# Kernel tuning notes

Measured on AMD Instinct MI355X. Metric: run time of the kernel, lower is better.

Reference implementation:

```python
import jax, jax.numpy as jnp
import numpy as np

B, S, D = 4, 2048, 1024
H, DK, DV, DFF = 16, 64, 64, 4096
EPS = 1e-5


def layer_norm(x, g, b):
    mu = jnp.mean(x, axis=-1, keepdims=True)
    var = jnp.mean((x - mu) ** 2, axis=-1, keepdims=True)
    return (x - mu) * jax.lax.rsqrt(var + EPS) * g + b


def setup_inputs() -> dict:
    key = jax.random.key(0)
    ks = jax.random.split(key, 12)
    s = lambda fan_in: 1.0 / np.sqrt(fan_in)
    return {
        "x": jax.random.normal(ks[0], (B, S, D), dtype=jnp.float32),
        # per-head projections stacked: [H, D, DK/DV] (x @ W layout)
        "Wq": jax.random.normal(ks[1], (H, D, DK), dtype=jnp.float32) * s(D),
        "Wk": jax.random.normal(ks[2], (H, D, DK), dtype=jnp.float32) * s(D),
        "Wv": jax.random.normal(ks[3], (H, D, DV), dtype=jnp.float32) * s(D),
        "Wo": jax.random.normal(ks[4], (H * DV, D), dtype=jnp.float32) * s(H * DV),
        "ln1_g": jnp.ones((D,), dtype=jnp.float32),
        "ln1_b": jnp.zeros((D,), dtype=jnp.float32),
        "W1": jax.random.normal(ks[5], (D, DFF), dtype=jnp.float32) * s(D),
        "b1": jnp.zeros((DFF,), dtype=jnp.float32),
        "W2": jax.random.normal(ks[6], (DFF, D), dtype=jnp.float32) * s(DFF),
        "b2": jnp.zeros((D,), dtype=jnp.float32),
        "ln2_g": jnp.ones((D,), dtype=jnp.float32),
        "ln2_b": jnp.zeros((D,), dtype=jnp.float32),
    }


def reference(x, Wq, Wk, Wv, Wo, ln1_g, ln1_b, W1, b1, W2, b2, ln2_g, ln2_b):
    # --- multi-head causal self-attention (all heads vectorized) ---
    q = jnp.einsum("bsd,hdk->bhsk", x, Wq)
    k = jnp.einsum("bsd,hdk->bhsk", x, Wk)
    v = jnp.einsum("bsd,hdv->bhsv", x, Wv)
    # NOTE: original scales by 1/sqrt(x.shape[-1]) == 1/sqrt(d_model)
    scale = 1.0 / np.sqrt(D).astype(np.float32)
    scores = jnp.einsum("bhsk,bhtk->bhst", q, k) * scale  # [B,H,S,S]
    causal = jnp.tril(jnp.ones((S, S), dtype=bool))
    scores = jnp.where(causal, scores, -jnp.inf)
    attn = jax.nn.softmax(scores, axis=-1)
    ctx = jnp.einsum("bhst,bhtv->bhsv", attn, v)  # [B,H,S,DV]
    # concat heads (head-major last dim, matches torch.cat order)
    ctx = ctx.transpose(0, 2, 1, 3).reshape(B, S, H * DV)
    attn_out = ctx @ Wo  # [B,S,D]
    # Sublayer 1 (dropout is identity in eval)
    h1 = layer_norm(x + attn_out, ln1_g, ln1_b)
    # --- FFN ---
    ff = jax.nn.relu(h1 @ W1 + b1) @ W2 + b2
    # Sublayer 2
    return layer_norm(h1 + ff, ln2_g, ln2_b)
```

## Files before the change

kernel.cpp:

```cpp
#include <hip/hip_runtime.h>

#define DEV __device__ __forceinline__

using f16x8 = _Float16 __attribute__((ext_vector_type(8)));
using f16x4 = _Float16 __attribute__((ext_vector_type(4)));
using f32x4 = float __attribute__((ext_vector_type(4)));

DEV f32x4 mfma16(f16x8 a, f16x8 b, f32x4 c) {
    return __builtin_amdgcn_mfma_f32_16x16x32_f16(a, b, c, 0, 0, 0);
}

DEV void gload16(const void* g, void* l) {
    __builtin_amdgcn_global_load_lds(
        (const __attribute__((address_space(1))) void*)g,
        (__attribute__((address_space(3))) void*)l, 16, 0, 0);
}

template <int MODE>
__global__ __launch_bounds__(256, 2) void gemm_bt(
    const _Float16* __restrict__ A, const _Float16* __restrict__ Bt,
    int M, int N, int K,
    const float* __restrict__ ep0, const float* __restrict__ ep1,
    void* __restrict__ o0, void* __restrict__ o1, void* __restrict__ o2)
{
    __shared__ __align__(16) _Float16 As[128 * 64];
    __shared__ __align__(16) _Float16 Bs[128 * 64];
    const int tid  = threadIdx.x;
    const int wave = tid >> 6, lane = tid & 63;
    const int l16  = lane & 15, g = lane >> 4;
    const int m0 = blockIdx.x * 128, n0 = blockIdx.y * 128;
    const int wm = (wave >> 1) * 64, wn = (wave & 1) * 64;

    f32x4 acc[4][4] = {};

    for (int kt = 0; kt < K; kt += 64) {
#pragma unroll
        for (int it = 0; it < 4; ++it) {
            const int off  = it * 4096 + tid * 16;
            const int row  = off >> 7;
            const int colb = (off & 127) ^ ((row & 7) << 4);
            gload16(A + (size_t)(m0 + row) * K + kt + (colb >> 1), (char*)As + off);
        }
#pragma unroll
        for (int it = 0; it < 4; ++it) {
            const int off  = it * 4096 + tid * 16;
            const int row  = off >> 7;
            const int colb = (off & 127) ^ ((row & 7) << 4);
            gload16(Bt + (size_t)(n0 + row) * K + kt + (colb >> 1), (char*)Bs + off);
        }
        __syncthreads();
#pragma unroll
        for (int kk = 0; kk < 2; ++kk) {
            f16x8 af[4], bfv[4];
#pragma unroll
            for (int i = 0; i < 4; ++i) {
                const int ar = wm + i * 16 + l16;
                const int cb = ((kk * 32 + g * 8) << 1) ^ ((ar & 7) << 4);
                af[i] = *(const f16x8*)((const char*)As + (ar << 7) + cb);
            }
#pragma unroll
            for (int j = 0; j < 4; ++j) {
                const int br = wn + j * 16 + l16;
                const int cb = ((kk * 32 + g * 8) << 1) ^ ((br & 7) << 4);
                bfv[j] = *(const f16x8*)((const char*)Bs + (br << 7) + cb);
            }
#pragma unroll
            for (int i = 0; i < 4; ++i)
#pragma unroll
                for (int j = 0; j < 4; ++j)
                    acc[i][j] = mfma16(af[i], bfv[j], acc[i][j]);
        }
        __syncthreads();
    }

#pragma unroll
    for (int i = 0; i < 4; ++i) {
#pragma unroll
        for (int j = 0; j < 4; ++j) {
#pragma unroll
            for (int r = 0; r < 4; ++r) {
                const int m = m0 + wm + i * 16 + g * 4 + r;
                const int n = n0 + wn + j * 16 + l16;
                const float val = acc[i][j][r];
                if constexpr (MODE == 0) {
                    const int b = m >> 11, s = m & 2047;
                    const int which = n >> 10, hh = (n >> 6) & 15, dd = n & 63;
                    const size_t bh = (size_t)(b * 16 + hh);
                    const _Float16 hv = (_Float16)val;
                    if (which == 0)      ((_Float16*)o0)[(bh * 2048 + s) * 64 + dd] = hv;
                    else if (which == 1) ((_Float16*)o1)[(bh * 2048 + s) * 64 + dd] = hv;
                    else                 ((_Float16*)o2)[(bh * 64 + dd) * 2048 + s] = hv;
                } else if constexpr (MODE == 1) {
                    const size_t idx = (size_t)m * N + n;
                    ((float*)o0)[idx] = val + ep0[idx];
                } else if constexpr (MODE == 2) {
                    float v = val + ep0[n];
                    ((_Float16*)o0)[(size_t)m * N + n] = (_Float16)(v > 0.f ? v : 0.f);
                } else {
                    const size_t idx = (size_t)m * N + n;
                    ((float*)o0)[idx] = val + ep0[n] + ep1[idx];
                }
            }
        }
    }
}

__global__ __launch_bounds__(256, 4) void attn_kernel(
    const _Float16* __restrict__ Q, const _Float16* __restrict__ Kb,
    const _Float16* __restrict__ Vt, _Float16* __restrict__ ctx)
{
    __shared__ __align__(16) _Float16 Ks[64 * 64];
    __shared__ __align__(16) _Float16 Vs[64 * 64];
    __shared__ __align__(16) _Float16 P_lds[4][16][72];
    __shared__ __align__(16) float f_lds[4][16];
    const int tid = threadIdx.x;
    const int w = tid >> 6, lane = tid & 63;
    const int l16 = lane & 15, g = lane >> 4;
    const int bh = blockIdx.y;
    const int b = bh >> 4, h = bh & 15;
    const int tA = blockIdx.x;

    const _Float16* Kh = Kb + (size_t)bh * 2048 * 64;
    const _Float16* Vh = Vt + (size_t)bh * 64 * 2048;
    const int swl = (l16 & 7) << 4;

    for (int half = 0; half < 2; ++half) {
        const int T = half ? (31 - tA) : tA;
        const int qbase = T * 64 + w * 16;
        const int qg = qbase + l16;

        const _Float16* qrow = Q + ((size_t)bh * 2048 + qg) * 64;
        const f16x8 qf0 = *(const f16x8*)(qrow + g * 8);
        const f16x8 qf1 = *(const f16x8*)(qrow + 32 + g * 8);

        f32x4 cacc[4] = {};
        float m_run = -INFINITY, l_run = 0.f;

        for (int kt = 0; kt <= T; ++kt) {
            const int kb0 = kt * 64;
#pragma unroll
            for (int it = 0; it < 2; ++it) {
                const int off  = it * 4096 + tid * 16;
                const int row  = off >> 7;
                const int colb = (off & 127) ^ ((row & 7) << 4);
                gload16(Kh + (size_t)(kb0 + row) * 64 + (colb >> 1), (char*)Ks + off);
            }
#pragma unroll
            for (int it = 0; it < 2; ++it) {
                const int off  = it * 4096 + tid * 16;
                const int row  = off >> 7;
                const int colb = (off & 127) ^ ((row & 7) << 4);
                gload16(Vh + (size_t)row * 2048 + kb0 + (colb >> 1), (char*)Vs + off);
            }
            __syncthreads();

            f32x4 st[4] = {{0.f,0.f,0.f,0.f},{0.f,0.f,0.f,0.f},
                           {0.f,0.f,0.f,0.f},{0.f,0.f,0.f,0.f}};
            __builtin_amdgcn_s_setprio(1);
#pragma unroll
            for (int s = 0; s < 4; ++s) {
                const char* kr = (const char*)Ks + (16 * s + l16) * 128;
                const f16x8 klo = *(const f16x8*)(kr + ((g * 16) ^ swl));
                const f16x8 khi = *(const f16x8*)(kr + ((64 + g * 16) ^ swl));
                st[s] = mfma16(klo, qf0, st[s]);
                st[s] = mfma16(khi, qf1, st[s]);
            }
            __builtin_amdgcn_s_setprio(0);

            const bool maskt = (kt == T);
            float sv[16];
            float tmax = -INFINITY;
#pragma unroll
            for (int s = 0; s < 4; ++s)
#pragma unroll
                for (int r = 0; r < 4; ++r) {
                    const int kg = kb0 + s * 16 + g * 4 + r;
                    float v = st[s][r] * 0.03125f;
                    v = (!maskt || kg <= qg) ? v : -INFINITY;
                    sv[s * 4 + r] = v;
                    tmax = fmaxf(tmax, v);
                }
            tmax = fmaxf(tmax, __shfl_xor(tmax, 16));
            tmax = fmaxf(tmax, __shfl_xor(tmax, 32));
            const float m_new = fmaxf(m_run, tmax);
            const float alpha = __expf(m_run - m_new);
            float tsum = 0.f;
            f16x4 p[4];
#pragma unroll
            for (int s = 0; s < 4; ++s)
#pragma unroll
                for (int r = 0; r < 4; ++r) {
                    const float e = __expf(sv[s * 4 + r] - m_new);
                    tsum += e;
                    p[s][r] = (_Float16)e;
                }
            tsum += __shfl_xor(tsum, 16);
            tsum += __shfl_xor(tsum, 32);
            l_run = l_run * alpha + tsum;
            m_run = m_new;

#pragma unroll
            for (int s = 0; s < 4; ++s)
                *(f16x4*)&P_lds[w][l16][s * 16 + g * 4] = p[s];
            if (g == 0) f_lds[w][l16] = alpha;

            const f32x4 al  = *(const f32x4*)&f_lds[w][g * 4];
            const f16x8 pf0 = *(const f16x8*)&P_lds[w][l16][g * 8];
            const f16x8 pf1 = *(const f16x8*)&P_lds[w][l16][32 + g * 8];
            __builtin_amdgcn_s_setprio(1);
#pragma unroll
            for (int jt = 0; jt < 4; ++jt) {
                const char* vr = (const char*)Vs + (jt * 16 + l16) * 128;
                const f16x8 vlo = *(const f16x8*)(vr + ((g * 16) ^ swl));
                const f16x8 vhi = *(const f16x8*)(vr + ((64 + g * 16) ^ swl));
#pragma unroll
                for (int r = 0; r < 4; ++r) cacc[jt][r] *= al[r];
                cacc[jt] = mfma16(pf0, vlo, cacc[jt]);
                cacc[jt] = mfma16(pf1, vhi, cacc[jt]);
            }
            __builtin_amdgcn_s_setprio(0);
            __syncthreads();
        }

        if (g == 0) f_lds[w][l16] = 1.f / l_run;
        const f32x4 il = *(const f32x4*)&f_lds[w][g * 4];
#pragma unroll
        for (int jt = 0; jt < 4; ++jt)
#pragma unroll
            for (int r = 0; r < 4; ++r)
                ctx[((size_t)b * 2048 + qbase + g * 4 + r) * 1024 + h * 64 + jt * 16 + l16]
                    = (_Float16)(cacc[jt][r] * il[r]);
    }
}

__global__ __launch_bounds__(256) void ln_kernel(
    const float* __restrict__ in, const float* __restrict__ gam, const float* __restrict__ bet,
    float* __restrict__ out32, _Float16* __restrict__ out16)
{
    const int row = blockIdx.x, tid = threadIdx.x;
    const float4 x = ((const float4*)(in + (size_t)row * 1024))[tid];
    float s  = x.x + x.y + x.z + x.w;
    float s2 = x.x * x.x + x.y * x.y + x.z * x.z + x.w * x.w;
#pragma unroll
    for (int o = 32; o > 0; o >>= 1) {
        s  += __shfl_xor(s, o);
        s2 += __shfl_xor(s2, o);
    }
    __shared__ float red[8];
    if ((tid & 63) == 0) { red[tid >> 6] = s; red[4 + (tid >> 6)] = s2; }
    __syncthreads();
    const float S  = red[0] + red[1] + red[2] + red[3];
    const float S2 = red[4] + red[5] + red[6] + red[7];
    const float mu = S * (1.f / 1024.f);
    const float ir = rsqrtf(S2 * (1.f / 1024.f) - mu * mu + 1e-5f);
    const float4 gv = ((const float4*)gam)[tid];
    const float4 bv = ((const float4*)bet)[tid];
    float4 o;
    o.x = (x.x - mu) * ir * gv.x + bv.x;
    o.y = (x.y - mu) * ir * gv.y + bv.y;
    o.z = (x.z - mu) * ir * gv.z + bv.z;
    o.w = (x.w - mu) * ir * gv.w + bv.w;
    if (out32) ((float4*)(out32 + (size_t)row * 1024))[tid] = o;
    if (out16) {
        f16x4 h;
        h[0] = (_Float16)o.x; h[1] = (_Float16)o.y; h[2] = (_Float16)o.z; h[3] = (_Float16)o.w;
        *(f16x4*)(out16 + (size_t)row * 1024 + tid * 4) = h;
    }
}

__global__ __launch_bounds__(256) void cast_f16(const float* __restrict__ in,
                                                _Float16* __restrict__ out, int n4)
{
    const int i = blockIdx.x * 256 + threadIdx.x;
    if (i < n4) {
        const float4 v = ((const float4*)in)[i];
        f16x4 h;
        h[0] = (_Float16)v.x; h[1] = (_Float16)v.y; h[2] = (_Float16)v.z; h[3] = (_Float16)v.w;
        ((f16x4*)out)[i] = h;
    }
}

__global__ __launch_bounds__(256) void transpose_cast(const float* __restrict__ src,
                                                      _Float16* __restrict__ dst, int K, int N)
{
    __shared__ float tile[64][65];
    const int n0 = blockIdx.x * 64, k0 = blockIdx.y * 64;
    const int tid = threadIdx.x;
#pragma unroll
    for (int it = 0; it < 16; ++it) {
        const int idx = it * 256 + tid;
        const int r = idx >> 6, c = idx & 63;
        tile[r][c] = src[(size_t)(k0 + r) * N + n0 + c];
    }
    __syncthreads();
#pragma unroll
    for (int it = 0; it < 16; ++it) {
        const int idx = it * 256 + tid;
        const int r = idx >> 6, c = idx & 63;
        dst[(size_t)(n0 + r) * K + k0 + c] = (_Float16)tile[c][r];
    }
}

__global__ __launch_bounds__(256) void pack_qkv_w(const float* __restrict__ Wq,
                                                  const float* __restrict__ Wk,
                                                  const float* __restrict__ Wv,
                                                  _Float16* __restrict__ dst)
{
    __shared__ float tile[64][65];
    const int n0 = blockIdx.x * 64, d0 = blockIdx.y * 64;
    const int which = n0 >> 10, hh = (n0 >> 6) & 15;
    const float* W = which == 0 ? Wq : (which == 1 ? Wk : Wv);
    const int tid = threadIdx.x;
#pragma unroll
    for (int it = 0; it < 16; ++it) {
        const int idx = it * 256 + tid;
        const int r = idx >> 6, c = idx & 63;
        tile[r][c] = W[((size_t)hh * 1024 + d0 + r) * 64 + c];
    }
    __syncthreads();
#pragma unroll
    for (int it = 0; it < 16; ++it) {
        const int idx = it * 256 + tid;
        const int r = idx >> 6, c = idx & 63;
        dst[(size_t)(n0 + r) * 1024 + d0 + c] = (_Float16)tile[c][r];
    }
}

extern "C" void kernel_launch(void* const* d_in, const int* in_sizes, int n_in,
                              void* d_out, int out_size, void* d_ws, size_t ws_size,
                              hipStream_t stream)
{
    const float* x    = (const float*)d_in[0];
    const float* Wq   = (const float*)d_in[1];
    const float* Wk   = (const float*)d_in[2];
    const float* Wv   = (const float*)d_in[3];
    const float* Wo   = (const float*)d_in[4];
    const float* ln1g = (const float*)d_in[5];
    const float* ln1b = (const float*)d_in[6];
    const float* W1   = (const float*)d_in[7];
    const float* b1   = (const float*)d_in[8];
    const float* W2   = (const float*)d_in[9];
    const float* b2   = (const float*)d_in[10];
    const float* ln2g = (const float*)d_in[11];
    const float* ln2b = (const float*)d_in[12];
    float* out = (float*)d_out;

    char* ws = (char*)d_ws;
    size_t off = 0;
    auto alloc = [&](size_t bytes) {
        void* p = ws + off;
        off += (bytes + 255) & ~(size_t)255;
        return p;
    };
    _Float16* x_h   = (_Float16*)alloc(8192ULL * 1024 * 2);
    _Float16* wqkv  = (_Float16*)alloc(3072ULL * 1024 * 2);
    _Float16* wo_t  = (_Float16*)alloc(1024ULL * 1024 * 2);
    _Float16* w1_t  = (_Float16*)alloc(4096ULL * 1024 * 2);
    _Float16* w2_t  = (_Float16*)alloc(1024ULL * 4096 * 2);
    _Float16* qbuf  = (_Float16*)alloc(8192ULL * 1024 * 2);
    _Float16* kbuf  = (_Float16*)alloc(8192ULL * 1024 * 2);
    _Float16* vt    = (_Float16*)alloc(8192ULL * 1024 * 2);
    _Float16* ctx   = (_Float16*)alloc(8192ULL * 1024 * 2);
    _Float16* ff1   = qbuf;
    float*    resid = (float*)alloc(8192ULL * 1024 * 4);
    float*    h1f   = (float*)alloc(8192ULL * 1024 * 4);
    _Float16* h1h   = (_Float16*)alloc(8192ULL * 1024 * 2);
    if (off > ws_size) return;

    cast_f16<<<8192, 256, 0, stream>>>(x, x_h, 2097152);
    pack_qkv_w<<<dim3(48, 16), 256, 0, stream>>>(Wq, Wk, Wv, wqkv);
    transpose_cast<<<dim3(16, 16), 256, 0, stream>>>(Wo, wo_t, 1024, 1024);
    transpose_cast<<<dim3(64, 16), 256, 0, stream>>>(W1, w1_t, 1024, 4096);
    transpose_cast<<<dim3(16, 64), 256, 0, stream>>>(W2, w2_t, 4096, 1024);

    gemm_bt<0><<<dim3(64, 24), 256, 0, stream>>>(x_h, wqkv, 8192, 3072, 1024,
                                                 nullptr, nullptr, qbuf, kbuf, vt);
    attn_kernel<<<dim3(16, 64), 256, 0, stream>>>(qbuf, kbuf, vt, ctx);
    gemm_bt<1><<<dim3(64, 8), 256, 0, stream>>>(ctx, wo_t, 8192, 1024, 1024,
                                                x, nullptr, resid, nullptr, nullptr);
    ln_kernel<<<8192, 256, 0, stream>>>(resid, ln1g, ln1b, h1f, h1h);
    gemm_bt<2><<<dim3(64, 32), 256, 0, stream>>>(h1h, w1_t, 8192, 4096, 1024,
                                                 b1, nullptr, ff1, nullptr, nullptr);
    gemm_bt<3><<<dim3(64, 8), 256, 0, stream>>>(ff1, w2_t, 8192, 1024, 4096,
                                                b2, h1f, resid, nullptr, nullptr);
    ln_kernel<<<8192, 256, 0, stream>>>(resid, ln2g, ln2b, out, nullptr);
}
```

Baseline: 387.1 us.

## Double attention KV tile to 128 keys and skip rescale when max unchanged

The attention kernel now processes 128 keys per iteration instead of 64, with larger K/V/P shared-memory tiles, a new V swizzle, and four MFMA steps per PV output. This halves the number of barriers and loop iterations per query tile. Accumulator rescaling is skipped whenever no row's running max increases. The P buffer is swizzled to reduce bank conflicts. The cost is more LDS per block and lower occupancy (3 blocks instead of 4), plus extra masked work on the diagonal tile, since a 128-key tile is only half valid when T is even.

```diff
diff --git a/kernel.cpp b/kernel.cpp
--- a/kernel.cpp
+++ b/kernel.cpp
@@ -105,13 +105,13 @@
     }
 }
 
-__global__ __launch_bounds__(256, 4) void attn_kernel(
+__global__ __launch_bounds__(256, 3) void attn_kernel(
     const _Float16* __restrict__ Q, const _Float16* __restrict__ Kb,
     const _Float16* __restrict__ Vt, _Float16* __restrict__ ctx)
 {
-    __shared__ __align__(16) _Float16 Ks[64 * 64];
-    __shared__ __align__(16) _Float16 Vs[64 * 64];
-    __shared__ __align__(16) _Float16 P_lds[4][16][72];
+    __shared__ __align__(16) _Float16 Ks[128 * 64];
+    __shared__ __align__(16) _Float16 Vs[64 * 128];
+    __shared__ __align__(16) _Float16 P_lds[4][16][128];
     __shared__ __align__(16) float f_lds[4][16];
     const int tid = threadIdx.x;
     const int w = tid >> 6, lane = tid & 63;
@@ -123,6 +123,7 @@
     const _Float16* Kh = Kb + (size_t)bh * 2048 * 64;
     const _Float16* Vh = Vt + (size_t)bh * 64 * 2048;
     const int swl = (l16 & 7) << 4;
+    const int swv = l16 << 4;
 
     for (int half = 0; half < 2; ++half) {
         const int T = half ? (31 - tA) : tA;
@@ -135,88 +136,100 @@
 
         f32x4 cacc[4] = {};
         float m_run = -INFINITY, l_run = 0.f;
-
-        for (int kt = 0; kt <= T; ++kt) {
-            const int kb0 = kt * 64;
-#pragma unroll
-            for (int it = 0; it < 2; ++it) {
+        const int nt = (T >> 1) + 1;
+
+        for (int kt = 0; kt < nt; ++kt) {
+            const int kb0 = kt << 7;
+#pragma unroll
+            for (int it = 0; it < 4; ++it) {
                 const int off  = it * 4096 + tid * 16;
                 const int row  = off >> 7;
                 const int colb = (off & 127) ^ ((row & 7) << 4);
                 gload16(Kh + (size_t)(kb0 + row) * 64 + (colb >> 1), (char*)Ks + off);
             }
 #pragma unroll
-            for (int it = 0; it < 2; ++it) {
+            for (int it = 0; it < 4; ++it) {
                 const int off  = it * 4096 + tid * 16;
-                const int row  = off >> 7;
-                const int colb = (off & 127) ^ ((row & 7) << 4);
+                const int row  = off >> 8;
+                const int colb = (off & 255) ^ ((row & 15) << 4);
                 gload16(Vh + (size_t)row * 2048 + kb0 + (colb >> 1), (char*)Vs + off);
             }
             __syncthreads();
 
-            f32x4 st[4] = {{0.f,0.f,0.f,0.f},{0.f,0.f,0.f,0.f},
-                           {0.f,0.f,0.f,0.f},{0.f,0.f,0.f,0.f}};
+            f32x4 st[8];
             __builtin_amdgcn_s_setprio(1);
 #pragma unroll
-            for (int s = 0; s < 4; ++s) {
+            for (int s = 0; s < 8; ++s) {
                 const char* kr = (const char*)Ks + (16 * s + l16) * 128;
                 const f16x8 klo = *(const f16x8*)(kr + ((g * 16) ^ swl));
                 const f16x8 khi = *(const f16x8*)(kr + ((64 + g * 16) ^ swl));
-                st[s] = mfma16(klo, qf0, st[s]);
-                st[s] = mfma16(khi, qf1, st[s]);
+                f32x4 a0 = {0.f, 0.f, 0.f, 0.f};
+                a0 = mfma16(klo, qf0, a0);
+                st[s] = mfma16(khi, qf1, a0);
             }
             __builtin_amdgcn_s_setprio(0);
 
-            const bool maskt = (kt == T);
-            float sv[16];
+            const bool maskt = (kt == nt - 1);
             float tmax = -INFINITY;
 #pragma unroll
-            for (int s = 0; s < 4; ++s)
+            for (int s = 0; s < 8; ++s)
 #pragma unroll
                 for (int r = 0; r < 4; ++r) {
                     const int kg = kb0 + s * 16 + g * 4 + r;
                     float v = st[s][r] * 0.03125f;
                     v = (!maskt || kg <= qg) ? v : -INFINITY;
-                    sv[s * 4 + r] = v;
+                    st[s][r] = v;
                     tmax = fmaxf(tmax, v);
                 }
             tmax = fmaxf(tmax, __shfl_xor(tmax, 16));
             tmax = fmaxf(tmax, __shfl_xor(tmax, 32));
-            const float m_new = fmaxf(m_run, tmax);
-            const float alpha = __expf(m_run - m_new);
+
+            if (__any(tmax > m_run)) {
+                const float m_new = fmaxf(m_run, tmax);
+                const float alpha = __expf(m_run - m_new);
+                m_run = m_new;
+                l_run *= alpha;
+                if (g == 0) f_lds[w][l16] = alpha;
+                const f32x4 al = *(const f32x4*)&f_lds[w][g * 4];
+#pragma unroll
+                for (int jt = 0; jt < 4; ++jt)
+#pragma unroll
+                    for (int r = 0; r < 4; ++r) cacc[jt][r] *= al[r];
+            }
+
             float tsum = 0.f;
-            f16x4 p[4];
-#pragma unroll
-            for (int s = 0; s < 4; ++s)
+            char* prow = (char*)&P_lds[w][l16][0];
+#pragma unroll
+            for (int s = 0; s < 8; ++s) {
+                f16x4 p;
 #pragma unroll
                 for (int r = 0; r < 4; ++r) {
-                    const float e = __expf(sv[s * 4 + r] - m_new);
+                    const float e = __expf(st[s][r] - m_run);
                     tsum += e;
-                    p[s][r] = (_Float16)e;
+                    p[r] = (_Float16)e;
                 }
+                *(f16x4*)(prow + ((s * 32 + g * 8) ^ swl)) = p;
+            }
             tsum += __shfl_xor(tsum, 16);
             tsum += __shfl_xor(tsum, 32);
-            l_run = l_run * alpha + tsum;
-            m_run = m_new;
-
-#pragma unroll
-            for (int s = 0; s < 4; ++s)
-                *(f16x4*)&P_lds[w][l16][s * 16 + g * 4] = p[s];
-            if (g == 0) f_lds[w][l16] = alpha;
-
-            const f32x4 al  = *(const f32x4*)&f_lds[w][g * 4];
-            const f16x8 pf0 = *(const f16x8*)&P_lds[w][l16][g * 8];
-            const f16x8 pf1 = *(const f16x8*)&P_lds[w][l16][32 + g * 8];
+            l_run += tsum;
+
+            const f16x8 pf0 = *(const f16x8*)(prow + ((g * 16) ^ swl));
+            const f16x8 pf1 = *(const f16x8*)(prow + ((64 + g * 16) ^ swl));
+            const f16x8 pf2 = *(const f16x8*)(prow + ((128 + g * 16) ^ swl));
+            const f16x8 pf3 = *(const f16x8*)(prow + ((192 + g * 16) ^ swl));
             __builtin_amdgcn_s_setprio(1);
 #pragma unroll
             for (int jt = 0; jt < 4; ++jt) {
-                const char* vr = (const char*)Vs + (jt * 16 + l16) * 128;
-                const f16x8 vlo = *(const f16x8*)(vr + ((g * 16) ^ swl));
-                const f16x8 vhi = *(const f16x8*)(vr + ((64 + g * 16) ^ swl));
-#pragma unroll
-                for (int r = 0; r < 4; ++r) cacc[jt][r] *= al[r];
-                cacc[jt] = mfma16(pf0, vlo, cacc[jt]);
-                cacc[jt] = mfma16(pf1, vhi, cacc[jt]);
+                const char* vr = (const char*)Vs + (jt * 16 + l16) * 256;
+                const f16x8 v0 = *(const f16x8*)(vr + ((g * 16) ^ swv));
+                const f16x8 v1 = *(const f16x8*)(vr + ((64 + g * 16) ^ swv));
+                const f16x8 v2 = *(const f16x8*)(vr + ((128 + g * 16) ^ swv));
+                const f16x8 v3 = *(const f16x8*)(vr + ((192 + g * 16) ^ swv));
+                cacc[jt] = mfma16(pf0, v0, cacc[jt]);
+                cacc[jt] = mfma16(pf1, v1, cacc[jt]);
+                cacc[jt] = mfma16(pf2, v2, cacc[jt]);
+                cacc[jt] = mfma16(pf3, v3, cacc[jt]);
             }
             __builtin_amdgcn_s_setprio(0);
             __syncthreads();
```

Measured after the change: 408.4 us. 1.06x slower.

## Double-buffer K/V tiles in attention and fold softmax scale into Q

Applied to the files above, without the earlier changes.

Attention now keeps two K/V tile buffers in LDS and prefetches tile kt+2 while computing tile kt, waiting with explicit vmcnt counts and raw barriers instead of a full __syncthreads each iteration. The softmax scale and log2(e) are folded into Q in the projection GEMM epilogue so the kernel can use exp2f without a per-score multiply. The output rescale is skipped when no row's max rises, alpha is passed by lane shuffles instead of LDS, and the P tile is stored with the swizzle. This costs more LDS per block, which may lower occupancy, and relies on a hand-counted vmcnt wait.

```diff
diff --git a/kernel.cpp b/kernel.cpp
--- a/kernel.cpp
+++ b/kernel.cpp
@@ -86,10 +86,14 @@
                     const int b = m >> 11, s = m & 2047;
                     const int which = n >> 10, hh = (n >> 6) & 15, dd = n & 63;
                     const size_t bh = (size_t)(b * 16 + hh);
-                    const _Float16 hv = (_Float16)val;
-                    if (which == 0)      ((_Float16*)o0)[(bh * 2048 + s) * 64 + dd] = hv;
-                    else if (which == 1) ((_Float16*)o1)[(bh * 2048 + s) * 64 + dd] = hv;
-                    else                 ((_Float16*)o2)[(bh * 64 + dd) * 2048 + s] = hv;
+                    if (which == 0) {
+                        ((_Float16*)o0)[(bh * 2048 + s) * 64 + dd] =
+                            (_Float16)(val * 0.04508422f);
+                    } else if (which == 1) {
+                        ((_Float16*)o1)[(bh * 2048 + s) * 64 + dd] = (_Float16)val;
+                    } else {
+                        ((_Float16*)o2)[(bh * 64 + dd) * 2048 + s] = (_Float16)val;
+                    }
                 } else if constexpr (MODE == 1) {
                     const size_t idx = (size_t)m * N + n;
                     ((float*)o0)[idx] = val + ep0[idx];
@@ -105,14 +109,30 @@
     }
 }
 
+DEV void stage_kv(const _Float16* __restrict__ Kh, const _Float16* __restrict__ Vh,
+                  int kb0, char* ksb, char* vsb, int tid)
+{
+#pragma unroll
+    for (int it = 0; it < 2; ++it) {
+        const int off  = it * 4096 + tid * 16;
+        const int row  = off >> 7;
+        const int colb = (off & 127) ^ ((row & 7) << 4);
+        gload16(Kh + (size_t)(kb0 + row) * 64 + (colb >> 1), ksb + off);
+    }
+#pragma unroll
+    for (int it = 0; it < 2; ++it) {
+        const int off  = it * 4096 + tid * 16;
+        const int row  = off >> 7;
+        const int colb = (off & 127) ^ ((row & 7) << 4);
+        gload16(Vh + (size_t)row * 2048 + kb0 + (colb >> 1), vsb + off);
+    }
+}
+
 __global__ __launch_bounds__(256, 4) void attn_kernel(
     const _Float16* __restrict__ Q, const _Float16* __restrict__ Kb,
     const _Float16* __restrict__ Vt, _Float16* __restrict__ ctx)
 {
-    __shared__ __align__(16) _Float16 Ks[64 * 64];
-    __shared__ __align__(16) _Float16 Vs[64 * 64];
-    __shared__ __align__(16) _Float16 P_lds[4][16][72];
-    __shared__ __align__(16) float f_lds[4][16];
+    __shared__ __align__(16) char smem[40960];
     const int tid = threadIdx.x;
     const int w = tid >> 6, lane = tid & 63;
     const int l16 = lane & 15, g = lane >> 4;
@@ -123,11 +143,13 @@
     const _Float16* Kh = Kb + (size_t)bh * 2048 * 64;
     const _Float16* Vh = Vt + (size_t)bh * 64 * 2048;
     const int swl = (l16 & 7) << 4;
+    char* prow = smem + 32768 + w * 2048 + l16 * 128;
 
     for (int half = 0; half < 2; ++half) {
         const int T = half ? (31 - tA) : tA;
         const int qbase = T * 64 + w * 16;
         const int qg = qbase + l16;
+        const int nt = T + 1;
 
         const _Float16* qrow = Q + ((size_t)bh * 2048 + qg) * 64;
         const f16x8 qf0 = *(const f16x8*)(qrow + g * 8);
@@ -136,94 +158,105 @@
         f32x4 cacc[4] = {};
         float m_run = -INFINITY, l_run = 0.f;
 
-        for (int kt = 0; kt <= T; ++kt) {
-            const int kb0 = kt * 64;
-#pragma unroll
-            for (int it = 0; it < 2; ++it) {
-                const int off  = it * 4096 + tid * 16;
-                const int row  = off >> 7;
-                const int colb = (off & 127) ^ ((row & 7) << 4);
-                gload16(Kh + (size_t)(kb0 + row) * 64 + (colb >> 1), (char*)Ks + off);
-            }
-#pragma unroll
-            for (int it = 0; it < 2; ++it) {
-                const int off  = it * 4096 + tid * 16;
-                const int row  = off >> 7;
-                const int colb = (off & 127) ^ ((row & 7) << 4);
-                gload16(Vh + (size_t)row * 2048 + kb0 + (colb >> 1), (char*)Vs + off);
-            }
-            __syncthreads();
-
-            f32x4 st[4] = {{0.f,0.f,0.f,0.f},{0.f,0.f,0.f,0.f},
-                           {0.f,0.f,0.f,0.f},{0.f,0.f,0.f,0.f}};
+        stage_kv(Kh, Vh, 0, smem, smem + 16384, tid);
+        if (nt > 1) stage_kv(Kh, Vh, 64, smem + 8192, smem + 24576, tid);
+
+        for (int kt = 0; kt < nt; ++kt) {
+            const int bufo = (kt & 1) << 13;
+            char* kbuf = smem + bufo;
+            char* vbuf = smem + 16384 + bufo;
+
+            if (kt + 1 < nt) asm volatile("s_waitcnt vmcnt(4)" ::: "memory");
+            else             asm volatile("s_waitcnt vmcnt(0)" ::: "memory");
+            __builtin_amdgcn_s_barrier();
+            __builtin_amdgcn_sched_barrier(0);
+
+            f32x4 st[4];
             __builtin_amdgcn_s_setprio(1);
 #pragma unroll
             for (int s = 0; s < 4; ++s) {
-                const char* kr = (const char*)Ks + (16 * s + l16) * 128;
+                const char* kr = kbuf + (16 * s + l16) * 128;
                 const f16x8 klo = *(const f16x8*)(kr + ((g * 16) ^ swl));
                 const f16x8 khi = *(const f16x8*)(kr + ((64 + g * 16) ^ swl));
-                st[s] = mfma16(klo, qf0, st[s]);
-                st[s] = mfma16(khi, qf1, st[s]);
+                f32x4 a0 = {0.f, 0.f, 0.f, 0.f};
+                a0 = mfma16(klo, qf0, a0);
+                st[s] = mfma16(khi, qf1, a0);
             }
             __builtin_amdgcn_s_setprio(0);
 
-            const bool maskt = (kt == T);
-            float sv[16];
-            float tmax = -INFINITY;
+            if (kt == nt - 1) {
+#pragma unroll
+                for (int s = 0; s < 4; ++s)
+#pragma unroll
+                    for (int r = 0; r < 4; ++r) {
+                        const int kg = kt * 64 + s * 16 + g * 4 + r;
+                        if (kg > qg) st[s][r] = -INFINITY;
+                    }
+            }
+
+            float tmax = st[0][0];
 #pragma unroll
             for (int s = 0; s < 4; ++s)
 #pragma unroll
-                for (int r = 0; r < 4; ++r) {
-                    const int kg = kb0 + s * 16 + g * 4 + r;
-                    float v = st[s][r] * 0.03125f;
-                    v = (!maskt || kg <= qg) ? v : -INFINITY;
-                    sv[s * 4 + r] = v;
-                    tmax = fmaxf(tmax, v);
-                }
+                for (int r = 0; r < 4; ++r) tmax = fmaxf(tmax, st[s][r]);
             tmax = fmaxf(tmax, __shfl_xor(tmax, 16));
             tmax = fmaxf(tmax, __shfl_xor(tmax, 32));
-            const float m_new = fmaxf(m_run, tmax);
-            const float alpha = __expf(m_run - m_new);
+
+            if (__any(tmax > m_run)) {
+                const float m_new = fmaxf(m_run, tmax);
+                const float alpha = exp2f(m_run - m_new);
+                m_run = m_new;
+                l_run *= alpha;
+                f32x4 al;
+#pragma unroll
+                for (int r = 0; r < 4; ++r) al[r] = __shfl(alpha, g * 4 + r);
+#pragma unroll
+                for (int jt = 0; jt < 4; ++jt)
+#pragma unroll
+                    for (int r = 0; r < 4; ++r) cacc[jt][r] *= al[r];
+            }
+
             float tsum = 0.f;
-            f16x4 p[4];
-#pragma unroll
-            for (int s = 0; s < 4; ++s)
+#pragma unroll
+            for (int s = 0; s < 4; ++s) {
+                f16x4 p;
 #pragma unroll
                 for (int r = 0; r < 4; ++r) {
-                    const float e = __expf(sv[s * 4 + r] - m_new);
+                    const float e = exp2f(st[s][r] - m_run);
                     tsum += e;
-                    p[s][r] = (_Float16)e;
+                    p[r] = (_Float16)e;
                 }
+                *(f16x4*)(prow + ((s * 32 + g * 8) ^ swl)) = p;
+            }
             tsum += __shfl_xor(tsum, 16);
             tsum += __shfl_xor(tsum, 32);
-            l_run = l_run * alpha + tsum;
-            m_run = m_new;
-
-#pragma unroll
-            for (int s = 0; s < 4; ++s)
-                *(f16x4*)&P_lds[w][l16][s * 16 + g * 4] = p[s];
-            if (g == 0) f_lds[w][l16] = alpha;
-
-            const f32x4 al  = *(const f32x4*)&f_lds[w][g * 4];
-            const f16x8 pf0 = *(const f16x8*)&P_lds[w][l16][g * 8];
-            const f16x8 pf1 = *(const f16x8*)&P_lds[w][l16][32 + g * 8];
+            l_run += tsum;
+
+            const f16x8 pf0 = *(const f16x8*)(prow + ((g * 16) ^ swl));
+            const f16x8 pf1 = *(const f16x8*)(prow + ((64 + g * 16) ^ swl));
             __builtin_amdgcn_s_setprio(1);
 #pragma unroll
             for (int jt = 0; jt < 4; ++jt) {
-                const char* vr = (const char*)Vs + (jt * 16 + l16) * 128;
+                const char* vr = vbuf + (jt * 16 + l16) * 128;
                 const f16x8 vlo = *(const f16x8*)(vr + ((g * 16) ^ swl));
                 const f16x8 vhi = *(const f16x8*)(vr + ((64 + g * 16) ^ swl));
-#pragma unroll
-                for (int r = 0; r < 4; ++r) cacc[jt][r] *= al[r];
                 cacc[jt] = mfma16(pf0, vlo, cacc[jt]);
                 cacc[jt] = mfma16(pf1, vhi, cacc[jt]);
             }
             __builtin_amdgcn_s_setprio(0);
-            __syncthreads();
+
+            __builtin_amdgcn_sched_barrier(0);
+            __builtin_amdgcn_s_barrier();
+            if (kt + 2 < nt)
+                stage_kv(Kh, Vh, (kt + 2) * 64, kbuf, vbuf, tid);
         }
 
-        if (g == 0) f_lds[w][l16] = 1.f / l_run;
-        const f32x4 il = *(const f32x4*)&f_lds[w][g * 4];
+        __builtin_amdgcn_s_barrier();
+
+        const float inv = 1.f / l_run;
+        f32x4 il;
+#pragma unroll
+        for (int r = 0; r < 4; ++r) il[r] = __shfl(inv, g * 4 + r);
 #pragma unroll
         for (int jt = 0; jt < 4; ++jt)
 #pragma unroll
```

Result: slower. 395.1 us (+2.1%).
